# Performance work log

Hardware: AMD Instinct MI355X
Metric: run time of the kernel (lower is better)

## Reference

```python
import jax, jax.numpy as jnp
import numpy as np

E, B, C = 4, 262144, 128  # edge types, tokens, feature dim

def setup_inputs() -> dict:
    key = jax.random.key(0)
    k1, k2, k3 = jax.random.split(key, 3)
    xs = jax.random.normal(k1, (E, B, C), dtype=jnp.float32)
    Ws = jax.random.normal(k2, (E, C, C), dtype=jnp.float32) * (1.0 / np.sqrt(C))
    bs = jax.random.normal(k3, (E, C), dtype=jnp.float32) * 0.01
    return {"xs": xs, "Ws": Ws, "bs": bs}

def reference(xs, Ws, bs):
    # Per-edge-type op: y_e = xs[e] @ Ws[e] + bs[e]  (Linear per from_node type)
    # Aggregation: sum over edges.
    # Fused grouped form: contract over edge axis e and input channel c in one einsum.
    out = jnp.einsum('ebc,ecd->bd', xs, Ws)          # [B, C]
    out = out + bs.sum(axis=0)                       # bias from each edge op, summed by aggregation
    return out
```

## Files before the change

kernel.cpp:

```cpp
#include <hip/hip_runtime.h>
#include <hip/hip_bf16.h>

#define N_E 4
#define N_B 262144
#define N_C 128

typedef __attribute__((ext_vector_type(8))) short bf16x8;
typedef __attribute__((ext_vector_type(4))) float f32x4;
typedef __attribute__((ext_vector_type(4))) unsigned int u32x4;

__device__ __forceinline__ unsigned pk2(float lo, float hi) {
  float2 t; t.x = lo; t.y = hi;
  __hip_bfloat162 h = __float22bfloat162_rn(t);
  union { __hip_bfloat162 h; unsigned u; } c;
  c.h = h;
  return c.u;
}

__global__ void __launch_bounds__(512, 2)
grouped_gemm(const float* __restrict__ xs, const float* __restrict__ Ws,
             const float* __restrict__ bs, float* __restrict__ out) {
  extern __shared__ unsigned char smem[];
  unsigned short* lds_w  = (unsigned short*)smem;
  float*          lds_bias = (float*)(smem + N_E * 16 * 128 * 16);

  const int tid  = threadIdx.x;
  const int lane = tid & 63;
  const int wave = tid >> 6;
  const int l15  = lane & 15;
  const int hi   = lane >> 4;

#pragma unroll
  for (int i = 0; i < 16; ++i) {
    int m = tid + i * 512;
    int e = m >> 11;
    int u = (m >> 7) & 15;
    int d = m & 127;
    const float* src = Ws + e * (N_C * N_C) + u * 8 * N_C + d;
    float v[8];
#pragma unroll
    for (int j = 0; j < 8; ++j) v[j] = src[j * N_C];
    u32x4 pk;
#pragma unroll
    for (int j = 0; j < 4; ++j) pk[j] = pk2(v[2 * j], v[2 * j + 1]);
    *reinterpret_cast<u32x4*>(&lds_w[(size_t)m * 8]) = pk;
  }
  if (tid < 128) {
    lds_bias[tid] = bs[tid] + bs[128 + tid] + bs[256 + tid] + bs[384 + tid];
  }
  __syncthreads();

  const int waveRow = blockIdx.x * 128 + wave * 16;

  f32x4 acc[8];
#pragma unroll
  for (int n = 0; n < 8; ++n) {
    f32x4 z = {0.0f, 0.0f, 0.0f, 0.0f};
    acc[n] = z;
  }

  const float* xrow = xs + (size_t)(waveRow + l15) * N_C;

#pragma unroll
  for (int e = 0; e < N_E; ++e) {
    const float* xe = xrow + (size_t)e * N_B * N_C;
#pragma unroll
    for (int kt = 0; kt < 4; ++kt) {
      const float* ap = xe + kt * 32 + hi * 8;
      f32x4 a0 = *reinterpret_cast<const f32x4*>(ap);
      f32x4 a1 = *reinterpret_cast<const f32x4*>(ap + 4);
      bf16x8 afrag;
      unsigned* au = reinterpret_cast<unsigned*>(&afrag);
      au[0] = pk2(a0[0], a0[1]);
      au[1] = pk2(a0[2], a0[3]);
      au[2] = pk2(a1[0], a1[1]);
      au[3] = pk2(a1[2], a1[3]);
      const unsigned short* wb = &lds_w[(size_t)((e * 16 + kt * 4 + hi) * 128 + l15) * 8];
#pragma unroll
      for (int n = 0; n < 8; ++n) {
        bf16x8 bfrag = *reinterpret_cast<const bf16x8*>(wb + (size_t)n * 16 * 8);
        acc[n] = __builtin_amdgcn_mfma_f32_16x16x32_bf16(afrag, bfrag, acc[n], 0, 0, 0);
      }
    }
  }

#pragma unroll
  for (int n = 0; n < 8; ++n) {
    int d = n * 16 + l15;
    float bias = lds_bias[d];
#pragma unroll
    for (int r = 0; r < 4; ++r) {
      int row = waveRow + hi * 4 + r;
      out[(size_t)row * N_C + d] = acc[n][r] + bias;
    }
  }
}

extern "C" void kernel_launch(void* const* d_in, const int* in_sizes, int n_in,
                              void* d_out, int out_size, void* d_ws, size_t ws_size,
                              hipStream_t stream) {
  const float* xs = (const float*)d_in[0];
  const float* Ws = (const float*)d_in[1];
  const float* bs = (const float*)d_in[2];
  float* out = (float*)d_out;

  const size_t smem = (size_t)N_E * 16 * 128 * 16 + 128 * sizeof(float);
  hipFuncSetAttribute((const void*)grouped_gemm,
                      hipFuncAttributeMaxDynamicSharedMemorySize, (int)smem);

  dim3 grid(N_B / 128);
  dim3 block(512);
  hipLaunchKernelGGL(grouped_gemm, grid, block, smem, stream, xs, Ws, bs, out);
}
```

Measured before the change: 163.8 us.

## Stage x tiles through LDS with async double-buffered global_load_lds

Activation rows are now copied into a per-wave, double-buffered, XOR-swizzled LDS region using asynchronous global-to-LDS loads issued two stages ahead. Waitcnt and sched barriers order the loads against the MFMA loop. This is meant to hide global memory latency behind the bf16 MFMA work in a bandwidth-bound kernel. Bias summation moves from LDS into per-thread registers. The extra LDS space and manual waitcnt handling add pressure and ordering risk.

```diff
diff --git a/kernel.cpp b/kernel.cpp
--- a/kernel.cpp
+++ b/kernel.cpp
@@ -17,18 +17,32 @@
   return c.u;
 }
 
+__device__ __forceinline__ void gload_lds16(const float* g, void* l) {
+  __builtin_amdgcn_global_load_lds((const __attribute__((address_space(1))) void*)g,
+                                   (__attribute__((address_space(3))) void*)l,
+                                   16, 0, 0);
+}
+
 __global__ void __launch_bounds__(512, 2)
 grouped_gemm(const float* __restrict__ xs, const float* __restrict__ Ws,
              const float* __restrict__ bs, float* __restrict__ out) {
   extern __shared__ unsigned char smem[];
-  unsigned short* lds_w  = (unsigned short*)smem;
-  float*          lds_bias = (float*)(smem + N_E * 16 * 128 * 16);
+  unsigned short* lds_w = (unsigned short*)smem;
+  unsigned char*  lds_a = smem + 131072;
 
   const int tid  = threadIdx.x;
   const int lane = tid & 63;
   const int wave = tid >> 6;
   const int l15  = lane & 15;
   const int hi   = lane >> 4;
+  const int waveRow = blockIdx.x * 128 + wave * 16;
+
+  float bias[8];
+#pragma unroll
+  for (int n = 0; n < 8; ++n) {
+    int d = n * 16 + l15;
+    bias[n] = bs[d] + bs[128 + d] + bs[256 + d] + bs[384 + d];
+  }
 
 #pragma unroll
   for (int i = 0; i < 16; ++i) {
@@ -45,12 +59,14 @@
     for (int j = 0; j < 4; ++j) pk[j] = pk2(v[2 * j], v[2 * j + 1]);
     *reinterpret_cast<u32x4*>(&lds_w[(size_t)m * 8]) = pk;
   }
-  if (tid < 128) {
-    lds_bias[tid] = bs[tid] + bs[128 + tid] + bs[256 + tid] + bs[384 + tid];
-  }
   __syncthreads();
 
-  const int waveRow = blockIdx.x * 128 + wave * 16;
+  const int r0 = lane >> 3;
+  const int wq = (((lane & 7) ^ r0) << 2);
+  const float* srcbase = xs + (size_t)(waveRow + r0) * N_C + wq;
+  unsigned char* abase = lds_a + wave * 4096;
+
+  const int rdoff = l15 * 128 + ((hi * 32) ^ ((l15 & 7) << 4));
 
   f32x4 acc[8];
 #pragma unroll
@@ -59,39 +75,58 @@
     acc[n] = z;
   }
 
-  const float* xrow = xs + (size_t)(waveRow + l15) * N_C;
+#define STAGE(s)                                                            \
+  do {                                                                      \
+    const float* g = srcbase + (size_t)((s) >> 2) * (N_B * N_C) + ((s) & 3) * 32; \
+    unsigned char* l = abase + ((s) & 1) * 2048;                            \
+    gload_lds16(g, l);                                                      \
+    gload_lds16(g + 8 * N_C, l + 1024);                                     \
+  } while (0)
+
+  STAGE(0);
+  STAGE(1);
 
 #pragma unroll
-  for (int e = 0; e < N_E; ++e) {
-    const float* xe = xrow + (size_t)e * N_B * N_C;
+  for (int s = 0; s < 16; ++s) {
+    const int e = s >> 2, kt = s & 3, b = s & 1;
+
+    if (s < 15) {
+      asm volatile("s_waitcnt vmcnt(2)" ::: "memory");
+    } else {
+      asm volatile("s_waitcnt vmcnt(0)" ::: "memory");
+    }
+    __builtin_amdgcn_sched_barrier(0);
+
+    const unsigned char* ab = abase + b * 2048;
+    f32x4 a0 = *reinterpret_cast<const f32x4*>(ab + rdoff);
+    f32x4 a1 = *reinterpret_cast<const f32x4*>(ab + (rdoff ^ 16));
+    bf16x8 afrag;
+    unsigned* au = reinterpret_cast<unsigned*>(&afrag);
+    au[0] = pk2(a0[0], a0[1]);
+    au[1] = pk2(a0[2], a0[3]);
+    au[2] = pk2(a1[0], a1[1]);
+    au[3] = pk2(a1[2], a1[3]);
+
+    asm volatile("s_waitcnt lgkmcnt(0)" ::: "memory");
+    __builtin_amdgcn_sched_barrier(0);
+    if (s < 14) STAGE(s + 2);
+
+    const unsigned short* wb = lds_w + (size_t)((e * 16 + kt * 4 + hi) * 128 + l15) * 8;
 #pragma unroll
-    for (int kt = 0; kt < 4; ++kt) {
-      const float* ap = xe + kt * 32 + hi * 8;
-      f32x4 a0 = *reinterpret_cast<const f32x4*>(ap);
-      f32x4 a1 = *reinterpret_cast<const f32x4*>(ap + 4);
-      bf16x8 afrag;
-      unsigned* au = reinterpret_cast<unsigned*>(&afrag);
-      au[0] = pk2(a0[0], a0[1]);
-      au[1] = pk2(a0[2], a0[3]);
-      au[2] = pk2(a1[0], a1[1]);
-      au[3] = pk2(a1[2], a1[3]);
-      const unsigned short* wb = &lds_w[(size_t)((e * 16 + kt * 4 + hi) * 128 + l15) * 8];
-#pragma unroll
-      for (int n = 0; n < 8; ++n) {
-        bf16x8 bfrag = *reinterpret_cast<const bf16x8*>(wb + (size_t)n * 16 * 8);
-        acc[n] = __builtin_amdgcn_mfma_f32_16x16x32_bf16(afrag, bfrag, acc[n], 0, 0, 0);
-      }
+    for (int n = 0; n < 8; ++n) {
+      bf16x8 bfrag = *reinterpret_cast<const bf16x8*>(wb + (size_t)n * 128);
+      acc[n] = __builtin_amdgcn_mfma_f32_16x16x32_bf16(afrag, bfrag, acc[n], 0, 0, 0);
     }
   }
+#undef STAGE
 
 #pragma unroll
   for (int n = 0; n < 8; ++n) {
     int d = n * 16 + l15;
-    float bias = lds_bias[d];
 #pragma unroll
     for (int r = 0; r < 4; ++r) {
       int row = waveRow + hi * 4 + r;
-      out[(size_t)row * N_C + d] = acc[n][r] + bias;
+      out[(size_t)row * N_C + d] = acc[n][r] + bias[n];
     }
   }
 }
@@ -104,7 +139,7 @@
   const float* bs = (const float*)d_in[2];
   float* out = (float*)d_out;
 
-  const size_t smem = (size_t)N_E * 16 * 128 * 16 + 128 * sizeof(float);
+  const size_t smem = 131072 + 32768;
   hipFuncSetAttribute((const void*)grouped_gemm,
                       hipFuncAttributeMaxDynamicSharedMemorySize, (int)smem);
 
```

Measured after the change: 155.0 us. -5.4%, faster.

## Software-pipeline activation loads with inline asm and double rows per block

Applied to the files above, without the earlier changes.

Replaces the compiler-scheduled loop with a 16-step unrolled schedule. Each step converts one pair of activation vectors while global loads for the chunk four steps ahead are already in flight, using inline-asm global_load_dwordx4 and explicit vmcnt waits. Blocks grow to 1024 threads covering 256 rows, so the fp32-to-bf16 conversion of the weights into LDS is paid over twice as many rows. The summed bias now lives in registers instead of LDS. The risks are that the inline asm and fixed vmcnt counts are fragile, and requesting 128KB of LDS may limit residency to one block per CU.

```diff
diff --git a/kernel.cpp b/kernel.cpp
--- a/kernel.cpp
+++ b/kernel.cpp
@@ -17,22 +17,29 @@
   return c.u;
 }
 
-__global__ void __launch_bounds__(512, 2)
+__global__ void __launch_bounds__(1024, 4)
 grouped_gemm(const float* __restrict__ xs, const float* __restrict__ Ws,
              const float* __restrict__ bs, float* __restrict__ out) {
   extern __shared__ unsigned char smem[];
-  unsigned short* lds_w  = (unsigned short*)smem;
-  float*          lds_bias = (float*)(smem + N_E * 16 * 128 * 16);
+  unsigned short* lds_w = (unsigned short*)smem;
 
   const int tid  = threadIdx.x;
   const int lane = tid & 63;
   const int wave = tid >> 6;
   const int l15  = lane & 15;
   const int hi   = lane >> 4;
+  const int waveRow = blockIdx.x * 256 + wave * 16;
+
+  float bias[8];
+#pragma unroll
+  for (int n = 0; n < 8; ++n) {
+    int d = n * 16 + l15;
+    bias[n] = bs[d] + bs[128 + d] + bs[256 + d] + bs[384 + d];
+  }
 
 #pragma unroll
-  for (int i = 0; i < 16; ++i) {
-    int m = tid + i * 512;
+  for (int i = 0; i < 8; ++i) {
+    int m = tid + i * 1024;
     int e = m >> 11;
     int u = (m >> 7) & 15;
     int d = m & 127;
@@ -45,12 +52,33 @@
     for (int j = 0; j < 4; ++j) pk[j] = pk2(v[2 * j], v[2 * j + 1]);
     *reinterpret_cast<u32x4*>(&lds_w[(size_t)m * 8]) = pk;
   }
-  if (tid < 128) {
-    lds_bias[tid] = bs[tid] + bs[128 + tid] + bs[256 + tid] + bs[384 + tid];
-  }
+
+  asm volatile("s_waitcnt vmcnt(0)" ::: "memory");
   __syncthreads();
 
-  const int waveRow = blockIdx.x * 128 + wave * 16;
+  const unsigned vb = (unsigned)(waveRow + l15) * 512u + (unsigned)hi * 32u;
+  const unsigned long long xbase = (unsigned long long)xs;
+
+  f32x4 A0[4], A1[4];
+
+#define AISSUE(c)                                                              \
+  do {                                                                         \
+    unsigned o;                                                                \
+    asm volatile("v_add_u32 %0, %1, %2"                                        \
+                 : "=v"(o)                                                     \
+                 : "n"(((c) >> 2) * 134217728u + ((c) & 3) * 128u), "v"(vb));  \
+    asm volatile("global_load_dwordx4 %0, %2, %3 offset:0\n\t"                 \
+                 "global_load_dwordx4 %1, %2, %3 offset:16"                    \
+                 : "=&v"(A0[(c) & 3]), "=&v"(A1[(c) & 3])                      \
+                 : "v"(o), "s"(xbase)                                          \
+                 : "memory");                                                  \
+  } while (0)
+
+#define WAITV(n)                                  \
+  do {                                            \
+    asm volatile("s_waitcnt vmcnt(" #n ")" ::: "memory"); \
+    __builtin_amdgcn_sched_barrier(0);            \
+  } while (0)
 
   f32x4 acc[8];
 #pragma unroll
@@ -59,39 +87,45 @@
     acc[n] = z;
   }
 
-  const float* xrow = xs + (size_t)(waveRow + l15) * N_C;
+  AISSUE(0); AISSUE(1); AISSUE(2); AISSUE(3);
 
-#pragma unroll
-  for (int e = 0; e < N_E; ++e) {
-    const float* xe = xrow + (size_t)e * N_B * N_C;
-#pragma unroll
-    for (int kt = 0; kt < 4; ++kt) {
-      const float* ap = xe + kt * 32 + hi * 8;
-      f32x4 a0 = *reinterpret_cast<const f32x4*>(ap);
-      f32x4 a1 = *reinterpret_cast<const f32x4*>(ap + 4);
-      bf16x8 afrag;
-      unsigned* au = reinterpret_cast<unsigned*>(&afrag);
-      au[0] = pk2(a0[0], a0[1]);
-      au[1] = pk2(a0[2], a0[3]);
-      au[2] = pk2(a1[0], a1[1]);
-      au[3] = pk2(a1[2], a1[3]);
-      const unsigned short* wb = &lds_w[(size_t)((e * 16 + kt * 4 + hi) * 128 + l15) * 8];
-#pragma unroll
-      for (int n = 0; n < 8; ++n) {
-        bf16x8 bfrag = *reinterpret_cast<const bf16x8*>(wb + (size_t)n * 16 * 8);
-        acc[n] = __builtin_amdgcn_mfma_f32_16x16x32_bf16(afrag, bfrag, acc[n], 0, 0, 0);
-      }
-    }
-  }
+#define STEP(s, w)                                                             \
+  do {                                                                         \
+    WAITV(w);                                                                  \
+    f32x4 a0 = A0[(s) & 3];                                                    \
+    f32x4 a1 = A1[(s) & 3];                                                    \
+    bf16x8 afrag;                                                              \
+    unsigned* au = reinterpret_cast<unsigned*>(&afrag);                        \
+    au[0] = pk2(a0[0], a0[1]);                                                 \
+    au[1] = pk2(a0[2], a0[3]);                                                 \
+    au[2] = pk2(a1[0], a1[1]);                                                 \
+    au[3] = pk2(a1[2], a1[3]);                                                 \
+    if ((s) <= 11) AISSUE((s) + 4);                                            \
+    const unsigned short* wb =                                                 \
+        lds_w + (size_t)((((s) >> 2) * 16 + ((s) & 3) * 4 + hi) * 128 + l15) * 8; \
+    _Pragma("unroll")                                                          \
+    for (int n = 0; n < 8; ++n) {                                              \
+      bf16x8 bfrag = *reinterpret_cast<const bf16x8*>(wb + (size_t)n * 128);   \
+      acc[n] = __builtin_amdgcn_mfma_f32_16x16x32_bf16(afrag, bfrag, acc[n], 0, 0, 0); \
+    }                                                                          \
+  } while (0)
+
+  STEP(0, 6);  STEP(1, 6);  STEP(2, 6);  STEP(3, 6);
+  STEP(4, 6);  STEP(5, 6);  STEP(6, 6);  STEP(7, 6);
+  STEP(8, 6);  STEP(9, 6);  STEP(10, 6); STEP(11, 6);
+  STEP(12, 6); STEP(13, 4); STEP(14, 2); STEP(15, 0);
+
+#undef STEP
+#undef WAITV
+#undef AISSUE
 
 #pragma unroll
   for (int n = 0; n < 8; ++n) {
     int d = n * 16 + l15;
-    float bias = lds_bias[d];
 #pragma unroll
     for (int r = 0; r < 4; ++r) {
       int row = waveRow + hi * 4 + r;
-      out[(size_t)row * N_C + d] = acc[n][r] + bias;
+      out[(size_t)row * N_C + d] = acc[n][r] + bias[n];
     }
   }
 }
@@ -104,11 +138,11 @@
   const float* bs = (const float*)d_in[2];
   float* out = (float*)d_out;
 
-  const size_t smem = (size_t)N_E * 16 * 128 * 16 + 128 * sizeof(float);
+  const size_t smem = 131072;
   hipFuncSetAttribute((const void*)grouped_gemm,
                       hipFuncAttributeMaxDynamicSharedMemorySize, (int)smem);
 
-  dim3 grid(N_B / 128);
-  dim3 block(512);
+  dim3 grid(N_B / 256);
+  dim3 block(1024);
   hipLaunchKernelGGL(grouped_gemm, grid, block, smem, stream, xs, Ws, bs, out);
 }
```

After: 145.9 us. 10.9% less time.
